# Kernel tuning notes

Measured on AMD Instinct MI355X. Metric: run time of the kernel, lower is better.

Reference implementation:

```python
import jax, jax.numpy as jnp
import numpy as np

L = 3            # max degree for L_in = L_edge = L_out = (0, 3)
B = 1024         # batch (number of edges)
C_IN = 256
C_OUT = 256
NUM_ORDERS = (L + 1) ** 2  # 16


def _build_structure(L):
    """Rebuild the coo_CG sparse structure: nonzeros sorted by (M_out, l1, l2),
    using the CG selection rule m1 + m2 = m for valid triangle triples."""
    triples = {}
    for l1 in range(L + 1):
        for l2 in range(L + 1):
            for l in range(abs(l1 - l2), min(L, l1 + l2) + 1):
                key = (l, l1, l2)
                if key not in triples:
                    triples[key] = len(triples)
    M1, M2, seg1, lind_g, seg2 = [], [], [], [], []
    g = 0
    for l in range(L + 1):
        for m in range(-l, l + 1):
            M = l * l + l + m  # flat order index of (l, m)
            for (lo, l1, l2) in sorted(triples.keys()):
                if lo != l:
                    continue
                cnt = 0
                for m1 in range(-l1, l1 + 1):
                    m2 = m - m1
                    if -l2 <= m2 <= l2:
                        M1.append(l1 * l1 + l1 + m1)
                        M2.append(l2 * l2 + l2 + m2)
                        seg1.append(g)
                        cnt += 1
                if cnt > 0:
                    lind_g.append(triples[(lo, l1, l2)])
                    seg2.append(M)
                    g += 1
    return (np.asarray(M1, np.int32), np.asarray(M2, np.int32),
            np.asarray(seg1, np.int32), np.asarray(lind_g, np.int32),
            np.asarray(seg2, np.int32), len(triples), g)


def setup_inputs() -> dict:
    key = jax.random.key(0)
    k1, k2, k3, k4 = jax.random.split(key, 4)
    M1, M2, seg1, l_ind, seg2, n_w, n_g = _build_structure(L)
    # expected: 478 nnz, 156 groups, 34 weights
    x = jax.random.normal(k1, (B, NUM_ORDERS, C_IN), jnp.float32)
    sh = jax.random.normal(k2, (B, NUM_ORDERS), jnp.float32)
    fan = np.sqrt(2.0 / (C_IN + C_OUT)).astype(np.float32)
    weight = jax.random.normal(k3, (n_w, C_IN, C_OUT), jnp.float32) * fan
    CG_vals = jax.random.normal(k4, (M1.shape[0],), jnp.float32) * 0.3
    return {
        'x': x, 'sh': sh, 'weight': weight, 'CG_vals': CG_vals,
        'M1': jnp.asarray(M1), 'M2': jnp.asarray(M2), 'seg1': jnp.asarray(seg1),
        'l_ind': jnp.asarray(l_ind), 'seg2': jnp.asarray(seg2),
        'num_orders_out': NUM_ORDERS,
    }


def reference(x, sh, weight, CG_vals, M1, M2, seg1, l_ind, seg2, num_orders_out):
    # x: (B, Mi, Ci); sh: (B, Me); weight: (num_weights, Ci, Co)
    Bn = x.shape[0]
    G = l_ind.shape[0]
    Ci = x.shape[-1]
    Co = weight.shape[-1]
    feat = x[:, M1, :]                                      # (B, nnz, Ci) gather on orders
    sh_g = sh[:, M2]                                        # (B, nnz)
    inter = (CG_vals[None, :] * sh_g)[..., None] * feat     # (B, nnz, Ci)
    inter = jnp.zeros((Bn, G, Ci), x.dtype).at[:, seg1, :].add(inter)   # segment over (M,l1,l2)
    w = weight[l_ind]                                       # (G, Ci, Co)
    ret = jnp.einsum('bgi,gio->bgo', inter, w)              # per-group matmul
    out = jnp.zeros((Bn, num_orders_out, Co), x.dtype).at[:, seg2, :].add(ret)  # segment over M
    return out
```

## Files before the change

kernel.cpp:

```cpp
#include <hip/hip_runtime.h>
#include <stdint.h>

#define B_SZ 1024
#define NO   16
#define CI   256
#define CO   256
#define BK   64
#define BM   32
#define LDB  72
#define LDAA 264
#define MAXG 12
#define MAXE 48
#define WP   76

typedef unsigned short u16;
typedef __attribute__((ext_vector_type(8))) short short8;
typedef __attribute__((ext_vector_type(4))) float f32x4;
typedef __attribute__((ext_vector_type(4))) unsigned short u16x4;
typedef __attribute__((ext_vector_type(8))) unsigned short u16x8;

__device__ __forceinline__ u16 f2bf(float f) {
  union { float f; uint32_t u; } v; v.f = f;
  uint32_t u = v.u;
  return (u16)((u + 0x7FFFu + ((u >> 16) & 1u)) >> 16);
}
__device__ __forceinline__ float bf2f(u16 h) {
  union { float f; uint32_t u; } v; v.u = ((uint32_t)h) << 16; return v.f;
}

__device__ __forceinline__ f32x4 mfma_16x16x32_bf16(short8 a, short8 b, f32x4 c) {
  asm volatile("v_mfma_f32_16x16x32_bf16 %0, %1, %2, %0" : "+v"(c) : "v"(a), "v"(b));
  return c;
}

extern "C" __global__ void xconv_kernel(const float* __restrict__ x,
                                        u16* __restrict__ xbf, int n8) {
  int t = blockIdx.x * 256 + threadIdx.x;
  if (t >= n8) return;
  const float* s = x + (size_t)t * 8;
  float4 a = ((const float4*)s)[0];
  float4 b = ((const float4*)s)[1];
  u16x8 pk;
  pk[0] = f2bf(a.x); pk[1] = f2bf(a.y); pk[2] = f2bf(a.z); pk[3] = f2bf(a.w);
  pk[4] = f2bf(b.x); pk[5] = f2bf(b.y); pk[6] = f2bf(b.z); pk[7] = f2bf(b.w);
  *(u16x8*)(xbf + (size_t)t * 8) = pk;
}

extern "C" __global__ void wconv_kernel(const float* __restrict__ w,
                                        u16* __restrict__ wbf) {
  __shared__ u16 t_lds[64 * WP];
  const int tid = threadIdx.x;
  const int bid = blockIdx.x;
  const int wi = bid >> 4;
  const int i0 = ((bid >> 2) & 3) * 64;
  const int o0 = (bid & 3) * 64;
  const float* src = w + (size_t)wi * (CI * CO);
  u16* dst = wbf + (size_t)wi * (CI * CO);
#pragma unroll
  for (int p = 0; p < 4; ++p) {
    int idx = p * 256 + tid;
    int i = idx >> 4, oq = (idx & 15) * 4;
    float4 v = *(const float4*)(src + (size_t)(i0 + i) * CO + o0 + oq);
    t_lds[(oq + 0) * WP + i] = f2bf(v.x);
    t_lds[(oq + 1) * WP + i] = f2bf(v.y);
    t_lds[(oq + 2) * WP + i] = f2bf(v.z);
    t_lds[(oq + 3) * WP + i] = f2bf(v.w);
  }
  __syncthreads();
#pragma unroll
  for (int p = 0; p < 4; ++p) {
    int idx = p * 256 + tid;
    int o = idx >> 4, iq = (idx & 15) * 4;
    u16x4 v;
    v[0] = t_lds[o * WP + iq + 0]; v[1] = t_lds[o * WP + iq + 1];
    v[2] = t_lds[o * WP + iq + 2]; v[3] = t_lds[o * WP + iq + 3];
    *(u16x4*)(dst + (size_t)(o0 + o) * CI + i0 + iq) = v;
  }
}

extern "C" __global__ void __launch_bounds__(256)
__attribute__((amdgpu_waves_per_eu(4, 4)))
so3_main(const u16* __restrict__ xbf,
         const float* __restrict__ sh,
         const float* __restrict__ CG,
         const u16* __restrict__ wbf,
         const int* __restrict__ M1,
         const int* __restrict__ M2,
         const int* __restrict__ seg1,
         const int* __restrict__ lind,
         const int* __restrict__ seg2,
         float* __restrict__ out,
         int G, int nnz) {
  __shared__ u16 As[BM * LDAA];
  __shared__ u16 Bs[128 * LDB];
  __shared__ u16 coefs[MAXE][BM];
  __shared__ int s_meta[4];
  __shared__ int s_estart[MAXG], s_eend[MAXG], s_wind[MAXG], s_m1[MAXE];

  const int tid = threadIdx.x;
  const int bid = blockIdx.x;
  const int b0  = (bid & 31) * BM;
  const int M   = (bid >> 5) & 15;
  const int co0 = (bid >> 9) * 128;

  if (tid == 0) { s_meta[0] = 1 << 30; s_meta[1] = 0; s_meta[2] = 1 << 30; s_meta[3] = 0; }
  if (tid < MAXG) { s_estart[tid] = 1 << 30; s_eend[tid] = 0; }
  if (tid < MAXE) s_m1[tid] = 0;
  __syncthreads();
  for (int g = tid; g < G; g += 256)
    if (seg2[g] == M) { atomicMin(&s_meta[0], g); atomicMax(&s_meta[1], g + 1); }
  __syncthreads();
  const int gstart = s_meta[0];
  const int ng = s_meta[1] - gstart;
  for (int e = tid; e < nnz; e += 256) {
    int g = seg1[e] - gstart;
    if (g >= 0 && g < ng) {
      atomicMin(&s_meta[2], e); atomicMax(&s_meta[3], e + 1);
      atomicMin(&s_estart[g], e); atomicMax(&s_eend[g], e + 1);
    }
  }
  __syncthreads();
  const int e0 = s_meta[2];
  const int ne = s_meta[3] - e0;
  for (int i = tid; i < ng; i += 256) s_wind[i] = lind[gstart + i];
  for (int i = tid; i < ne; i += 256) s_m1[i] = M1[e0 + i];
  for (int idx = tid; idx < ne * BM; idx += 256) {
    int el = idx / BM, r = idx & (BM - 1);
    int e = e0 + el;
    coefs[el][r] = f2bf(CG[e] * sh[(size_t)(b0 + r) * NO + M2[e]]);
  }
  __syncthreads();

  const int lane = tid & 63;
  const int wn = tid >> 6;
  const int lrow = lane & 15, lq = lane >> 4;
  const int ar = tid >> 3;
  const int ak = (tid & 7) * 8;

  f32x4 acc[2][2];
#pragma unroll
  for (int i = 0; i < 2; ++i)
#pragma unroll
    for (int j = 0; j < 2; ++j) acc[i][j] = (f32x4){0.f, 0.f, 0.f, 0.f};

  const int T = ng * 4;

  auto buildA = [&](int gl) {
    const int ea = s_estart[gl] - e0;
    const int cnt = (s_eend[gl] - e0) - ea;
    const u16* xb = xbf + (size_t)(b0 + ar) * (NO * CI) + ak;
    float cf[8]; int mo[8];
    const int mo0 = s_m1[ea] * CI;
#pragma unroll
    for (int j = 0; j < 8; ++j) {
      bool v = j < cnt;
      cf[j] = v ? bf2f(coefs[ea + j][ar]) : 0.f;
      mo[j] = v ? s_m1[ea + j] * CI : mo0;
    }
#pragma unroll
    for (int h = 0; h < 2; ++h) {
      float ax[2][8];
#pragma unroll
      for (int q = 0; q < 2; ++q)
#pragma unroll
        for (int j = 0; j < 8; ++j) ax[q][j] = 0.f;
#pragma unroll
      for (int p = 0; p < 4; ++p) {
        if (2 * p < cnt) {
          u16x8 vX[2], vY[2];
#pragma unroll
          for (int q = 0; q < 2; ++q) vX[q] = *(const u16x8*)(xb + mo[2 * p] + (2 * h + q) * 64);
#pragma unroll
          for (int q = 0; q < 2; ++q) vY[q] = *(const u16x8*)(xb + mo[2 * p + 1] + (2 * h + q) * 64);
          const float c0 = cf[2 * p], c1 = cf[2 * p + 1];
#pragma unroll
          for (int q = 0; q < 2; ++q)
#pragma unroll
            for (int j = 0; j < 8; ++j)
              ax[q][j] = fmaf(c1, bf2f((u16)vY[q][j]),
                         fmaf(c0, bf2f((u16)vX[q][j]), ax[q][j]));
        }
      }
#pragma unroll
      for (int q = 0; q < 2; ++q) {
        u16x8 pk;
#pragma unroll
        for (int j = 0; j < 8; ++j) pk[j] = f2bf(ax[q][j]);
        *(u16x8*)&As[ar * LDAA + (2 * h + q) * 64 + ak] = pk;
      }
    }
  };

  u16x8 breg[4];
  {
    const u16* wb = wbf + (size_t)s_wind[0] * (CI * CO) + (size_t)co0 * CI;
#pragma unroll
    for (int rr = 0; rr < 4; ++rr) {
      int idx = tid + rr * 256, o = idx >> 3, ic = (idx & 7) * 8;
      breg[rr] = *(const u16x8*)(wb + (size_t)o * CI + ic);
    }
  }

  for (int t = 0; t < T; ++t) {
    const int gl = t >> 2, kk = t & 3;
    if (kk == 0) buildA(gl);
#pragma unroll
    for (int rr = 0; rr < 4; ++rr) {
      int idx = tid + rr * 256, o = idx >> 3, ic = (idx & 7) * 8;
      *(u16x8*)&Bs[o * LDB + ic] = breg[rr];
    }
    {
      int tn = (t + 1 < T) ? t + 1 : t;
      int gln = tn >> 2, kkn = (tn & 3) * BK;
      const u16* wbn = wbf + (size_t)s_wind[gln] * (CI * CO) + (size_t)co0 * CI + kkn;
#pragma unroll
      for (int rr = 0; rr < 4; ++rr) {
        int idx = tid + rr * 256, o = idx >> 3, ic = (idx & 7) * 8;
        breg[rr] = *(const u16x8*)(wbn + (size_t)o * CI + ic);
      }
    }
    __syncthreads();
#pragma unroll
    for (int ks = 0; ks < 2; ++ks) {
      short8 af[2], bfr[2];
#pragma unroll
      for (int mf = 0; mf < 2; ++mf)
        af[mf] = *(const short8*)&As[(mf * 16 + lrow) * LDAA + kk * 64 + ks * 32 + lq * 8];
#pragma unroll
      for (int nf = 0; nf < 2; ++nf)
        bfr[nf] = *(const short8*)&Bs[(wn * 32 + nf * 16 + lrow) * LDB + ks * 32 + lq * 8];
#pragma unroll
      for (int mf = 0; mf < 2; ++mf)
#pragma unroll
        for (int nf = 0; nf < 2; ++nf)
          acc[mf][nf] = mfma_16x16x32_bf16(af[mf], bfr[nf], acc[mf][nf]);
    }
    __syncthreads();
  }

#pragma unroll
  for (int mf = 0; mf < 2; ++mf) {
    int brow = b0 + mf * 16 + lq * 4;
#pragma unroll
    for (int nf = 0; nf < 2; ++nf) {
      int o = co0 + wn * 32 + nf * 16 + lrow;
#pragma unroll
      for (int rg = 0; rg < 4; ++rg)
        out[(size_t)(brow + rg) * (NO * CO) + (size_t)M * CO + o] = acc[mf][nf][rg];
    }
  }
}

extern "C" void kernel_launch(void* const* d_in, const int* in_sizes, int n_in,
                              void* d_out, int out_size, void* d_ws, size_t ws_size,
                              hipStream_t stream) {
  const float* x   = (const float*)d_in[0];
  const float* sh  = (const float*)d_in[1];
  const float* wgt = (const float*)d_in[2];
  const float* CG  = (const float*)d_in[3];
  const int* M1    = (const int*)d_in[4];
  const int* M2    = (const int*)d_in[5];
  const int* seg1  = (const int*)d_in[6];
  const int* lind  = (const int*)d_in[7];
  const int* seg2  = (const int*)d_in[8];
  float* out       = (float*)d_out;

  const int nnz = in_sizes[3];
  const int G   = in_sizes[7];
  const int n_w = in_sizes[2] / (CI * CO);

  u16* xbf = (u16*)d_ws;
  u16* wbf = (u16*)((char*)d_ws + (size_t)B_SZ * NO * CI * 2);

  int n8 = B_SZ * NO * CI / 8;
  xconv_kernel<<<dim3(n8 / 256), dim3(256), 0, stream>>>(x, xbf, n8);
  wconv_kernel<<<dim3(n_w * 16), dim3(256), 0, stream>>>(wgt, wbf);
  so3_main<<<dim3(1024), dim3(256), 0, stream>>>(xbf, sh, CG, wbf, M1, M2, seg1, lind, seg2,
                                                 out, G, nnz);
}
```

Baseline: 162.2 us.

## Make weight tile staging wave-private to drop per-k-step block barriers

Each wave now loads and stores only its own 32 output-channel rows of the weight tile into a private slice of the shared buffer, instead of the whole block cooperatively staging the full tile. Because no other wave reads that slice, the two block-wide barriers per k-step are removed. Barriers now surround only the per-group A-tile build, two per group instead of eight. This relies on a wave's own LDS writes and reads staying ordered, and it keeps the register prefetch of the next B chunk.

```diff
diff --git a/kernel.cpp b/kernel.cpp
--- a/kernel.cpp
+++ b/kernel.cpp
@@ -136,14 +136,13 @@
   const int lrow = lane & 15, lq = lane >> 4;
   const int ar = tid >> 3;
   const int ak = (tid & 7) * 8;
+  u16* bsw = &Bs[wn * 32 * LDB];
 
   f32x4 acc[2][2];
 #pragma unroll
   for (int i = 0; i < 2; ++i)
 #pragma unroll
     for (int j = 0; j < 2; ++j) acc[i][j] = (f32x4){0.f, 0.f, 0.f, 0.f};
-
-  const int T = ng * 4;
 
   auto buildA = [&](int gl) {
     const int ea = s_estart[gl] - e0;
@@ -192,50 +191,50 @@
   };
 
   u16x8 breg[4];
-  {
-    const u16* wb = wbf + (size_t)s_wind[0] * (CI * CO) + (size_t)co0 * CI;
+  auto loadB = [&](int gl, int kkB) {
+    const u16* wbn = wbf + (size_t)s_wind[gl] * (CI * CO)
+                   + (size_t)(co0 + wn * 32) * CI + kkB;
 #pragma unroll
     for (int rr = 0; rr < 4; ++rr) {
-      int idx = tid + rr * 256, o = idx >> 3, ic = (idx & 7) * 8;
-      breg[rr] = *(const u16x8*)(wb + (size_t)o * CI + ic);
-    }
-  }
-
-  for (int t = 0; t < T; ++t) {
-    const int gl = t >> 2, kk = t & 3;
-    if (kk == 0) buildA(gl);
-#pragma unroll
-    for (int rr = 0; rr < 4; ++rr) {
-      int idx = tid + rr * 256, o = idx >> 3, ic = (idx & 7) * 8;
-      *(u16x8*)&Bs[o * LDB + ic] = breg[rr];
-    }
-    {
-      int tn = (t + 1 < T) ? t + 1 : t;
-      int gln = tn >> 2, kkn = (tn & 3) * BK;
-      const u16* wbn = wbf + (size_t)s_wind[gln] * (CI * CO) + (size_t)co0 * CI + kkn;
+      int idx = lane + rr * 64, o = idx >> 3, ic = (idx & 7) * 8;
+      breg[rr] = *(const u16x8*)(wbn + (size_t)o * CI + ic);
+    }
+  };
+
+  loadB(0, 0);
+  const int T = ng * 4;
+
+  for (int gl = 0; gl < ng; ++gl) {
+    __syncthreads();
+    buildA(gl);
+    __syncthreads();
+#pragma unroll
+    for (int kk = 0; kk < 4; ++kk) {
 #pragma unroll
       for (int rr = 0; rr < 4; ++rr) {
-        int idx = tid + rr * 256, o = idx >> 3, ic = (idx & 7) * 8;
-        breg[rr] = *(const u16x8*)(wbn + (size_t)o * CI + ic);
-      }
-    }
-    __syncthreads();
-#pragma unroll
-    for (int ks = 0; ks < 2; ++ks) {
-      short8 af[2], bfr[2];
-#pragma unroll
-      for (int mf = 0; mf < 2; ++mf)
-        af[mf] = *(const short8*)&As[(mf * 16 + lrow) * LDAA + kk * 64 + ks * 32 + lq * 8];
-#pragma unroll
-      for (int nf = 0; nf < 2; ++nf)
-        bfr[nf] = *(const short8*)&Bs[(wn * 32 + nf * 16 + lrow) * LDB + ks * 32 + lq * 8];
-#pragma unroll
-      for (int mf = 0; mf < 2; ++mf)
+        int idx = lane + rr * 64, o = idx >> 3, ic = (idx & 7) * 8;
+        *(u16x8*)&bsw[o * LDB + ic] = breg[rr];
+      }
+      {
+        int tn = gl * 4 + kk + 1; if (tn >= T) tn = T - 1;
+        loadB(tn >> 2, (tn & 3) * BK);
+      }
+#pragma unroll
+      for (int ks = 0; ks < 2; ++ks) {
+        short8 af[2], bfr[2];
+#pragma unroll
+        for (int mf = 0; mf < 2; ++mf)
+          af[mf] = *(const short8*)&As[(mf * 16 + lrow) * LDAA + kk * 64 + ks * 32 + lq * 8];
 #pragma unroll
         for (int nf = 0; nf < 2; ++nf)
-          acc[mf][nf] = mfma_16x16x32_bf16(af[mf], bfr[nf], acc[mf][nf]);
-    }
-    __syncthreads();
+          bfr[nf] = *(const short8*)&bsw[(nf * 16 + lrow) * LDB + ks * 32 + lq * 8];
+#pragma unroll
+        for (int mf = 0; mf < 2; ++mf)
+#pragma unroll
+          for (int nf = 0; nf < 2; ++nf)
+            acc[mf][nf] = mfma_16x16x32_bf16(af[mf], bfr[nf], acc[mf][nf]);
+      }
+    }
   }
 
 #pragma unroll
```

Measured after the change: 159.0 us. About the same (-1.9%).
